# Kernel tuning notes

Hardware: AMD Instinct MI355X
Metric: run time of the kernel (lower is better)

## Reference

```python
import jax, jax.numpy as jnp
import numpy as np

B, NU, NI, D, L = 8, 1024, 2048, 64, 2
NUM_USERS, NUM_ITEMS = 100000, 50000


def setup_inputs() -> dict:
    key = jax.random.key(0)
    ks = jax.random.split(key, 9)
    return {
        "user_indices": jax.random.randint(ks[0], (B, NU), 0, NUM_USERS),
        "item_indices": jax.random.randint(ks[1], (B, NI), 0, NUM_ITEMS),
        "adj_matrices": jax.random.uniform(ks[2], (B, NU + NI, NU + NI), dtype=jnp.float32),
        "user_table": jax.random.normal(ks[3], (NUM_USERS, D), dtype=jnp.float32),
        "item_table": jax.random.normal(ks[4], (NUM_ITEMS, D), dtype=jnp.float32),
        "gc_w": jax.random.normal(ks[5], (L, D, D), dtype=jnp.float32) * 0.05,
        "gc_b": jax.random.normal(ks[6], (L, D), dtype=jnp.float32) * 0.05,
        "bi_w": jax.random.normal(ks[7], (L, D, D), dtype=jnp.float32) * 0.05,
        "bi_b": jax.random.normal(ks[8], (L, D), dtype=jnp.float32) * 0.05,
    }


def reference(user_indices, item_indices, adj_matrices, user_table, item_table, gc_w, gc_b, bi_w, bi_b):
    n_layers = gc_w.shape[0]

    def per_sample(u_idx, i_idx, adj):
        u_emb = user_table[u_idx]            # [NU, D]
        i_emb = item_table[i_idx]            # [NI, D]
        ego = jnp.concatenate([u_emb, i_emb], axis=0)  # [N, D]
        all_embs = [ego]
        for l in range(n_layers):
            side = adj @ ego                                        # [N, D]
            s = jax.nn.leaky_relu(side @ gc_w[l].T + gc_b[l])       # Linear(out,in) -> x @ W.T + b
            bi = jax.nn.leaky_relu((ego * side) @ bi_w[l].T + bi_b[l])
            ego = s + bi
            all_embs.append(ego)
        all_e = jnp.concatenate(all_embs, axis=1)                   # [N, D*(L+1)]
        u_g, i_g = all_e[: u_emb.shape[0]], all_e[u_emb.shape[0]:]
        scores = u_g @ i_g.T                                        # [NU, NI]
        return jax.nn.log_softmax(scores, axis=1)

    return jax.vmap(per_sample)(user_indices, item_indices, adj_matrices)
```

## Files before the change

kernel.cpp:

```cpp
#include <hip/hip_runtime.h>
#include <cstddef>

#define BB   8
#define NUU  1024
#define NII  2048
#define NTOT 3072
#define DD   64
#define KCAT 192

typedef __attribute__((ext_vector_type(8))) short bf16x8;
typedef __attribute__((ext_vector_type(4))) float f32x4;

__device__ __forceinline__ unsigned short f2bf(float f) {
  unsigned u = __float_as_uint(f);
  return (unsigned short)((u + 0x7fffu + ((u >> 16) & 1u)) >> 16);
}
__device__ __forceinline__ float bf2f(unsigned short s) {
  return __uint_as_float(((unsigned)s) << 16);
}
__device__ __forceinline__ uint4 pack8(float4 a, float4 b) {
  uint4 r;
  r.x = (unsigned)f2bf(a.x) | ((unsigned)f2bf(a.y) << 16);
  r.y = (unsigned)f2bf(a.z) | ((unsigned)f2bf(a.w) << 16);
  r.z = (unsigned)f2bf(b.x) | ((unsigned)f2bf(b.y) << 16);
  r.w = (unsigned)f2bf(b.z) | ((unsigned)f2bf(b.w) << 16);
  return r;
}
__device__ __forceinline__ bf16x8 u4_to_bf(uint4 u) {
  union { uint4 a; bf16x8 b; } x; x.a = u; return x.b;
}

__global__ __launch_bounds__(256) void transpose_w(
    const float* __restrict__ gcw, const float* __restrict__ biw,
    float* __restrict__ wT) {
  int g = blockIdx.x * 256 + threadIdx.x;
  int m = g >> 12, r = g & 4095;
  int k = r >> 6, d = r & 63;
  const float* src = (m < 2) ? gcw + m * 4096 : biw + (m - 2) * 4096;
  wT[g] = src[d * 64 + k];
}

__global__ __launch_bounds__(256) void gather_bf16(
    const int* __restrict__ uidx, const int* __restrict__ iidx,
    const float* __restrict__ utab, const float* __restrict__ itab,
    unsigned short* __restrict__ ecat) {
  int g = blockIdx.x * 256 + threadIdx.x;
  int node_g = g >> 2;
  int f0 = (g & 3) * 16;
  int b = node_g / NTOT;
  int row = node_g - b * NTOT;
  const float* src = (row < NUU) ? utab + (size_t)uidx[b * NUU + row] * DD
                                 : itab + (size_t)iidx[b * NII + row - NUU] * DD;
  const float4* s4 = reinterpret_cast<const float4*>(src + f0);
  uint4 lo = pack8(s4[0], s4[1]);
  uint4 hi = pack8(s4[2], s4[3]);
  uint4* dst = reinterpret_cast<uint4*>(ecat + (size_t)node_g * KCAT + f0);
  dst[0] = lo; dst[1] = hi;
}

__global__ __launch_bounds__(256) void conv_t(
    const unsigned short* __restrict__ ecat, int c0,
    unsigned short* __restrict__ Et) {
  __shared__ unsigned short T[64][65];
  const int tid = threadIdx.x;
  const int b = blockIdx.y;
  const int r0 = blockIdx.x * 64;
  {
    int nl = tid >> 2, fg = (tid & 3) * 16;
    const uint4* src = reinterpret_cast<const uint4*>(
        ecat + ((size_t)b * NTOT + r0 + nl) * KCAT + c0 + fg);
    uint4 v0 = src[0], v1 = src[1];
    unsigned short tmp[16];
    *reinterpret_cast<uint4*>(tmp) = v0;
    *reinterpret_cast<uint4*>(tmp + 8) = v1;
#pragma unroll
    for (int j = 0; j < 16; j++) T[fg + j][nl] = tmp[j];
  }
  __syncthreads();
  {
    int f = tid >> 2, ng = (tid & 3) * 16;
    unsigned short tmp[16];
#pragma unroll
    for (int j = 0; j < 16; j++) tmp[j] = T[f][ng + j];
    uint4* dst = reinterpret_cast<uint4*>(
        Et + ((size_t)b * DD + f) * NTOT + r0 + ng);
    dst[0] = *reinterpret_cast<uint4*>(tmp);
    dst[1] = *reinterpret_cast<uint4*>(tmp + 8);
  }
}

template <int CONV>
__global__ __launch_bounds__(256) void side_mfma_t(
    const float* __restrict__ adj, unsigned short* __restrict__ adjb,
    const unsigned short* __restrict__ Et, float* __restrict__ sp) {
  __shared__ __align__(16) unsigned short Bs[2][64][68];
  const int tid = threadIdx.x;
  const int w = tid >> 6, l = tid & 63;
  const int lane15 = l & 15, quad = l >> 4;
  const int b = blockIdx.z, kz = blockIdx.y;
  const int m0 = blockIdx.x * 64 + w * 16;
  const int kbase = kz * 768;
  const size_t rowoff = (size_t)b * NTOT * NTOT +
                        (size_t)(m0 + lane15) * NTOT + kbase + quad * 8;
  const float* A32 = adj + rowoff;
  const unsigned short* A16 = adjb + rowoff;
  unsigned short* Aw = adjb + rowoff;

  const int sf = tid >> 3, ss = (tid & 7) * 8;
  const unsigned short* Eb = Et + (size_t)b * DD * NTOT + kbase;
  uint4 p0 = *reinterpret_cast<const uint4*>(Eb + (size_t)sf * NTOT + ss);
  uint4 p1 = *reinterpret_cast<const uint4*>(Eb + (size_t)(sf + 32) * NTOT + ss);

  bf16x8 a0, a1;
  float4 f0, f1, f2, f3;
  if (CONV) {
    f0 = *reinterpret_cast<const float4*>(A32 + 0);
    f1 = *reinterpret_cast<const float4*>(A32 + 4);
    f2 = *reinterpret_cast<const float4*>(A32 + 32);
    f3 = *reinterpret_cast<const float4*>(A32 + 36);
  } else {
    a0 = *reinterpret_cast<const bf16x8*>(A16);
    a1 = *reinterpret_cast<const bf16x8*>(A16 + 32);
  }

  f32x4 acc[4];
#pragma unroll
  for (int t = 0; t < 4; t++) acc[t] = (f32x4){0.f, 0.f, 0.f, 0.f};

  for (int c = 0; c < 12; c++) {
    const int buf = c & 1;
    __syncthreads();
    *reinterpret_cast<uint4*>(&Bs[buf][sf][ss]) = p0;
    *reinterpret_cast<uint4*>(&Bs[buf][sf + 32][ss]) = p1;
    __syncthreads();

    if (CONV) {
      uint4 u0 = pack8(f0, f1), u1 = pack8(f2, f3);
      *reinterpret_cast<uint4*>(Aw + c * 64) = u0;
      *reinterpret_cast<uint4*>(Aw + c * 64 + 32) = u1;
      a0 = u4_to_bf(u0);
      a1 = u4_to_bf(u1);
    }

    bf16x8 na0, na1;
    if (c + 1 < 12) {
      p0 = *reinterpret_cast<const uint4*>(Eb + (size_t)sf * NTOT + (c + 1) * 64 + ss);
      p1 = *reinterpret_cast<const uint4*>(Eb + (size_t)(sf + 32) * NTOT + (c + 1) * 64 + ss);
      if (CONV) {
        f0 = *reinterpret_cast<const float4*>(A32 + (c + 1) * 64);
        f1 = *reinterpret_cast<const float4*>(A32 + (c + 1) * 64 + 4);
        f2 = *reinterpret_cast<const float4*>(A32 + (c + 1) * 64 + 32);
        f3 = *reinterpret_cast<const float4*>(A32 + (c + 1) * 64 + 36);
      } else {
        na0 = *reinterpret_cast<const bf16x8*>(A16 + (c + 1) * 64);
        na1 = *reinterpret_cast<const bf16x8*>(A16 + (c + 1) * 64 + 32);
      }
    }

#pragma unroll
    for (int t = 0; t < 4; t++) {
      bf16x8 b0 = *reinterpret_cast<const bf16x8*>(&Bs[buf][t * 16 + lane15][quad * 8]);
      acc[t] = __builtin_amdgcn_mfma_f32_16x16x32_bf16(a0, b0, acc[t], 0, 0, 0);
    }
#pragma unroll
    for (int t = 0; t < 4; t++) {
      bf16x8 b1 = *reinterpret_cast<const bf16x8*>(&Bs[buf][t * 16 + lane15][32 + quad * 8]);
      acc[t] = __builtin_amdgcn_mfma_f32_16x16x32_bf16(a1, b1, acc[t], 0, 0, 0);
    }
    if (!CONV && (c + 1 < 12)) { a0 = na0; a1 = na1; }
  }

  float* S = sp + ((size_t)kz * BB + b) * ((size_t)NTOT * DD);
#pragma unroll
  for (int t = 0; t < 4; t++)
#pragma unroll
    for (int r = 0; r < 4; r++)
      S[(size_t)(m0 + quad * 4 + r) * DD + t * 16 + lane15] = acc[t][r];
}

__global__ __launch_bounds__(256) void layer_post(
    const float* __restrict__ sp, unsigned short* __restrict__ ecat, int cin,
    const float* __restrict__ wTg, const float* __restrict__ wTb,
    const float* __restrict__ gcb, const float* __restrict__ bib) {
  __shared__ float wG[4096];
  __shared__ float wB[4096];
  __shared__ float rowS[4][64];
  __shared__ float rowE[4][64];
  const int tid = threadIdx.x;
#pragma unroll
  for (int i = 0; i < 16; i++) {
    int idx = tid + i * 256;
    wG[idx] = wTg[idx];
    wB[idx] = wTb[idx];
  }
  const int wv = tid >> 6, lane = tid & 63;
  const size_t row = (size_t)blockIdx.x * 4 + wv;
  const size_t off = row * DD + lane;
  const size_t P = (size_t)BB * NTOT * DD;
  float sv = sp[off] + sp[P + off] + sp[2 * P + off] + sp[3 * P + off];
  float ev = bf2f(ecat[row * KCAT + cin + lane]);
  rowS[wv][lane] = sv;
  rowE[wv][lane] = ev;
  __syncthreads();
  float sacc = gcb[lane];
  float bacc = bib[lane];
#pragma unroll 8
  for (int k = 0; k < 64; k++) {
    float sk = rowS[wv][k];
    float ek = rowE[wv][k];
    sacc += sk * wG[k * 64 + lane];
    bacc += (ek * sk) * wB[k * 64 + lane];
  }
  float s  = sacc > 0.f ? sacc : 0.01f * sacc;
  float bi = bacc > 0.f ? bacc : 0.01f * bacc;
  ecat[row * KCAT + cin + 64 + lane] = f2bf(s + bi);
}

__global__ __launch_bounds__(256) void scores_mfma(
    const unsigned short* __restrict__ ecat, float* __restrict__ out) {
  __shared__ __align__(16) unsigned short Ut[64 * KCAT];
  __shared__ __align__(16) unsigned short It[64 * KCAT];
  const int tid = threadIdx.x;
  const int w = tid >> 6, l = tid & 63;
  const int lane15 = l & 15, quad = l >> 4;
  const int b = blockIdx.z;
  const int u0 = blockIdx.y * 64;
  const int i0 = blockIdx.x * 64;
#pragma unroll
  for (int it = 0; it < 6; it++) {
    int idx = tid + it * 256;
    int row = idx / 24, c = idx - row * 24;
    int cs = c ^ (row & 7);
    uint4 vu = reinterpret_cast<const uint4*>(
        ecat + ((size_t)b * NTOT + u0 + row) * KCAT)[c];
    uint4 vi = reinterpret_cast<const uint4*>(
        ecat + ((size_t)b * NTOT + NUU + i0 + row) * KCAT)[c];
    reinterpret_cast<uint4*>(Ut)[row * 24 + cs] = vu;
    reinterpret_cast<uint4*>(It)[row * 24 + cs] = vi;
  }
  __syncthreads();
  f32x4 acc[4];
#pragma unroll
  for (int t = 0; t < 4; t++) acc[t] = (f32x4){0.f, 0.f, 0.f, 0.f};
  const int urow = w * 16 + lane15;
#pragma unroll
  for (int ks = 0; ks < 6; ks++) {
    int cu = (ks * 4 + quad) ^ (urow & 7);
    bf16x8 af = reinterpret_cast<const bf16x8*>(Ut)[urow * 24 + cu];
#pragma unroll
    for (int t = 0; t < 4; t++) {
      int irow = t * 16 + lane15;
      int ci = (ks * 4 + quad) ^ (irow & 7);
      bf16x8 bf = reinterpret_cast<const bf16x8*>(It)[irow * 24 + ci];
      acc[t] = __builtin_amdgcn_mfma_f32_16x16x32_bf16(af, bf, acc[t], 0, 0, 0);
    }
  }
  float* O = out + (size_t)b * NUU * NII;
#pragma unroll
  for (int t = 0; t < 4; t++)
#pragma unroll
    for (int r = 0; r < 4; r++)
      O[(size_t)(u0 + w * 16 + quad * 4 + r) * NII + i0 + t * 16 + lane15] =
          acc[t][r];
}

__global__ __launch_bounds__(256) void logsoftmax_kernel(float* __restrict__ out) {
  __shared__ float rm[4];
  __shared__ float rs[4];
  const int tid = threadIdx.x;
  const int lane = tid & 63, wv = tid >> 6;
  float* row = out + (size_t)blockIdx.x * NII;
  float4 v0 = *reinterpret_cast<const float4*>(row + tid * 4);
  float4 v1 = *reinterpret_cast<const float4*>(row + 1024 + tid * 4);
  float m = fmaxf(fmaxf(fmaxf(v0.x, v0.y), fmaxf(v0.z, v0.w)),
                  fmaxf(fmaxf(v1.x, v1.y), fmaxf(v1.z, v1.w)));
#pragma unroll
  for (int off = 32; off > 0; off >>= 1) m = fmaxf(m, __shfl_xor(m, off));
  if (lane == 0) rm[wv] = m;
  __syncthreads();
  m = fmaxf(fmaxf(rm[0], rm[1]), fmaxf(rm[2], rm[3]));
  float s = expf(v0.x - m) + expf(v0.y - m) + expf(v0.z - m) + expf(v0.w - m) +
            expf(v1.x - m) + expf(v1.y - m) + expf(v1.z - m) + expf(v1.w - m);
#pragma unroll
  for (int off = 32; off > 0; off >>= 1) s += __shfl_xor(s, off);
  if (lane == 0) rs[wv] = s;
  __syncthreads();
  float lse = m + logf(rs[0] + rs[1] + rs[2] + rs[3]);
  v0.x -= lse; v0.y -= lse; v0.z -= lse; v0.w -= lse;
  v1.x -= lse; v1.y -= lse; v1.z -= lse; v1.w -= lse;
  *reinterpret_cast<float4*>(row + tid * 4) = v0;
  *reinterpret_cast<float4*>(row + 1024 + tid * 4) = v1;
}

extern "C" void kernel_launch(void* const* d_in, const int* in_sizes, int n_in,
                              void* d_out, int out_size, void* d_ws, size_t ws_size,
                              hipStream_t stream) {
  (void)in_sizes; (void)n_in; (void)out_size; (void)ws_size;
  const int*   uidx = (const int*)d_in[0];
  const int*   iidx = (const int*)d_in[1];
  const float* adj  = (const float*)d_in[2];
  const float* utab = (const float*)d_in[3];
  const float* itab = (const float*)d_in[4];
  const float* gcw  = (const float*)d_in[5];
  const float* gcb  = (const float*)d_in[6];
  const float* biw  = (const float*)d_in[7];
  const float* bib  = (const float*)d_in[8];
  float* out = (float*)d_out;

  unsigned short* ecat = (unsigned short*)d_ws;
  unsigned short* Et   = ecat + (size_t)BB * NTOT * KCAT;
  unsigned short* adjb = Et + (size_t)BB * DD * NTOT;
  float* sp = (float*)d_out;
  const size_t P = (size_t)BB * NTOT * DD;
  float* wT = (float*)d_out + 4 * P;

  transpose_w<<<dim3(64), 256, 0, stream>>>(gcw, biw, wT);
  gather_bf16<<<dim3(BB * NTOT * 4 / 256), 256, 0, stream>>>(uidx, iidx, utab, itab, ecat);
  conv_t<<<dim3(48, BB), 256, 0, stream>>>(ecat, 0, Et);
  side_mfma_t<1><<<dim3(48, 4, BB), 256, 0, stream>>>(adj, adjb, Et, sp);
  layer_post<<<dim3(BB * NTOT / 4), 256, 0, stream>>>(sp, ecat, 0, wT, wT + 2 * 4096, gcb, bib);
  conv_t<<<dim3(48, BB), 256, 0, stream>>>(ecat, 64, Et);
  side_mfma_t<0><<<dim3(48, 4, BB), 256, 0, stream>>>(adj, adjb, Et, sp);
  layer_post<<<dim3(BB * NTOT / 4), 256, 0, stream>>>(sp, ecat, 64, wT + 4096, wT + 3 * 4096, gcb + 64, bib + 64);
  scores_mfma<<<dim3(32, 16, BB), 256, 0, stream>>>(ecat, out);
  logsoftmax_kernel<<<dim3(BB * NUU), 256, 0, stream>>>(out);
}
```

Measured before the change: 629.3 us.

## Fuse gather, transpose and weight prep; halve split-K; batch rows in layer_post

The embedding gather, the first bf16 transpose and the weight transpose now run in one kernel, which removes two launches and one round trip of ecat through global memory. The side GEMM's split-K factor drops from 4 to 2, so each block covers twice as many K chunks and fewer partial sums are written and reduced, at the cost of fewer blocks and longer serial loops. layer_post now handles 16 rows per block, four per wave, so the shared-memory weights are loaded fewer times and each weight read is reused across four rows.

```diff
diff --git a/kernel.cpp b/kernel.cpp
--- a/kernel.cpp
+++ b/kernel.cpp
@@ -30,32 +30,52 @@
   union { uint4 a; bf16x8 b; } x; x.a = u; return x.b;
 }
 
-__global__ __launch_bounds__(256) void transpose_w(
-    const float* __restrict__ gcw, const float* __restrict__ biw,
-    float* __restrict__ wT) {
-  int g = blockIdx.x * 256 + threadIdx.x;
-  int m = g >> 12, r = g & 4095;
-  int k = r >> 6, d = r & 63;
-  const float* src = (m < 2) ? gcw + m * 4096 : biw + (m - 2) * 4096;
-  wT[g] = src[d * 64 + k];
-}
-
-__global__ __launch_bounds__(256) void gather_bf16(
+__global__ __launch_bounds__(256) void gather_t(
     const int* __restrict__ uidx, const int* __restrict__ iidx,
     const float* __restrict__ utab, const float* __restrict__ itab,
-    unsigned short* __restrict__ ecat) {
-  int g = blockIdx.x * 256 + threadIdx.x;
-  int node_g = g >> 2;
-  int f0 = (g & 3) * 16;
-  int b = node_g / NTOT;
-  int row = node_g - b * NTOT;
-  const float* src = (row < NUU) ? utab + (size_t)uidx[b * NUU + row] * DD
-                                 : itab + (size_t)iidx[b * NII + row - NUU] * DD;
-  const float4* s4 = reinterpret_cast<const float4*>(src + f0);
-  uint4 lo = pack8(s4[0], s4[1]);
-  uint4 hi = pack8(s4[2], s4[3]);
-  uint4* dst = reinterpret_cast<uint4*>(ecat + (size_t)node_g * KCAT + f0);
-  dst[0] = lo; dst[1] = hi;
+    const float* __restrict__ gcw, const float* __restrict__ biw,
+    unsigned short* __restrict__ ecat, unsigned short* __restrict__ Et,
+    float* __restrict__ wT) {
+  const int tid = threadIdx.x;
+  if (blockIdx.x >= 384) {
+    for (int i = tid; i < 16384; i += 256) {
+      int m = i >> 12, r = i & 4095;
+      int k = r >> 6, d = r & 63;
+      const float* src = (m < 2) ? gcw + m * 4096 : biw + (m - 2) * 4096;
+      wT[i] = src[d * 64 + k];
+    }
+    return;
+  }
+  __shared__ unsigned short T[64][65];
+  const int b = blockIdx.x / 48;
+  const int r0 = (blockIdx.x % 48) * 64;
+  {
+    int nl = tid >> 2, f0 = (tid & 3) * 16;
+    int row = r0 + nl;
+    const float* src = (row < NUU) ? utab + (size_t)uidx[b * NUU + row] * DD
+                                   : itab + (size_t)iidx[b * NII + row - NUU] * DD;
+    const float4* s4 = reinterpret_cast<const float4*>(src + f0);
+    uint4 lo = pack8(s4[0], s4[1]);
+    uint4 hi = pack8(s4[2], s4[3]);
+    uint4* dst = reinterpret_cast<uint4*>(ecat + ((size_t)b * NTOT + row) * KCAT + f0);
+    dst[0] = lo; dst[1] = hi;
+    unsigned short tmp[16];
+    *reinterpret_cast<uint4*>(tmp) = lo;
+    *reinterpret_cast<uint4*>(tmp + 8) = hi;
+#pragma unroll
+    for (int j = 0; j < 16; j++) T[f0 + j][nl] = tmp[j];
+  }
+  __syncthreads();
+  {
+    int f = tid >> 2, ng = (tid & 3) * 16;
+    unsigned short tmp[16];
+#pragma unroll
+    for (int j = 0; j < 16; j++) tmp[j] = T[f][ng + j];
+    uint4* dst = reinterpret_cast<uint4*>(
+        Et + ((size_t)b * DD + f) * NTOT + r0 + ng);
+    dst[0] = *reinterpret_cast<uint4*>(tmp);
+    dst[1] = *reinterpret_cast<uint4*>(tmp + 8);
+  }
 }
 
 __global__ __launch_bounds__(256) void conv_t(
@@ -99,7 +119,7 @@
   const int lane15 = l & 15, quad = l >> 4;
   const int b = blockIdx.z, kz = blockIdx.y;
   const int m0 = blockIdx.x * 64 + w * 16;
-  const int kbase = kz * 768;
+  const int kbase = kz * 1536;
   const size_t rowoff = (size_t)b * NTOT * NTOT +
                         (size_t)(m0 + lane15) * NTOT + kbase + quad * 8;
   const float* A32 = adj + rowoff;
@@ -127,7 +147,7 @@
 #pragma unroll
   for (int t = 0; t < 4; t++) acc[t] = (f32x4){0.f, 0.f, 0.f, 0.f};
 
-  for (int c = 0; c < 12; c++) {
+  for (int c = 0; c < 24; c++) {
     const int buf = c & 1;
     __syncthreads();
     *reinterpret_cast<uint4*>(&Bs[buf][sf][ss]) = p0;
@@ -143,7 +163,7 @@
     }
 
     bf16x8 na0, na1;
-    if (c + 1 < 12) {
+    if (c + 1 < 24) {
       p0 = *reinterpret_cast<const uint4*>(Eb + (size_t)sf * NTOT + (c + 1) * 64 + ss);
       p1 = *reinterpret_cast<const uint4*>(Eb + (size_t)(sf + 32) * NTOT + (c + 1) * 64 + ss);
       if (CONV) {
@@ -167,7 +187,7 @@
       bf16x8 b1 = *reinterpret_cast<const bf16x8*>(&Bs[buf][t * 16 + lane15][32 + quad * 8]);
       acc[t] = __builtin_amdgcn_mfma_f32_16x16x32_bf16(a1, b1, acc[t], 0, 0, 0);
     }
-    if (!CONV && (c + 1 < 12)) { a0 = na0; a1 = na1; }
+    if (!CONV && (c + 1 < 24)) { a0 = na0; a1 = na1; }
   }
 
   float* S = sp + ((size_t)kz * BB + b) * ((size_t)NTOT * DD);
@@ -184,8 +204,8 @@
     const float* __restrict__ gcb, const float* __restrict__ bib) {
   __shared__ float wG[4096];
   __shared__ float wB[4096];
-  __shared__ float rowS[4][64];
-  __shared__ float rowE[4][64];
+  __shared__ float rowS[16][64];
+  __shared__ float rowE[16][64];
   const int tid = threadIdx.x;
 #pragma unroll
   for (int i = 0; i < 16; i++) {
@@ -194,26 +214,38 @@
     wB[idx] = wTb[idx];
   }
   const int wv = tid >> 6, lane = tid & 63;
-  const size_t row = (size_t)blockIdx.x * 4 + wv;
-  const size_t off = row * DD + lane;
+  const size_t base = (size_t)blockIdx.x * 16;
   const size_t P = (size_t)BB * NTOT * DD;
-  float sv = sp[off] + sp[P + off] + sp[2 * P + off] + sp[3 * P + off];
-  float ev = bf2f(ecat[row * KCAT + cin + lane]);
-  rowS[wv][lane] = sv;
-  rowE[wv][lane] = ev;
-  __syncthreads();
-  float sacc = gcb[lane];
-  float bacc = bib[lane];
+#pragma unroll
+  for (int rr = 0; rr < 4; rr++) {
+    const size_t row = base + wv * 4 + rr;
+    const size_t off = row * DD + lane;
+    rowS[wv * 4 + rr][lane] = sp[off] + sp[P + off];
+    rowE[wv * 4 + rr][lane] = bf2f(ecat[row * KCAT + cin + lane]);
+  }
+  __syncthreads();
+  float sacc[4], bacc[4];
+#pragma unroll
+  for (int rr = 0; rr < 4; rr++) { sacc[rr] = gcb[lane]; bacc[rr] = bib[lane]; }
 #pragma unroll 8
   for (int k = 0; k < 64; k++) {
-    float sk = rowS[wv][k];
-    float ek = rowE[wv][k];
-    sacc += sk * wG[k * 64 + lane];
-    bacc += (ek * sk) * wB[k * 64 + lane];
-  }
-  float s  = sacc > 0.f ? sacc : 0.01f * sacc;
-  float bi = bacc > 0.f ? bacc : 0.01f * bacc;
-  ecat[row * KCAT + cin + 64 + lane] = f2bf(s + bi);
+    float wg = wG[k * 64 + lane];
+    float wb = wB[k * 64 + lane];
+#pragma unroll
+    for (int rr = 0; rr < 4; rr++) {
+      float sk = rowS[wv * 4 + rr][k];
+      float ek = rowE[wv * 4 + rr][k];
+      sacc[rr] += sk * wg;
+      bacc[rr] += (ek * sk) * wb;
+    }
+  }
+#pragma unroll
+  for (int rr = 0; rr < 4; rr++) {
+    float s  = sacc[rr] > 0.f ? sacc[rr] : 0.01f * sacc[rr];
+    float bi = bacc[rr] > 0.f ? bacc[rr] : 0.01f * bacc[rr];
+    const size_t row = base + wv * 4 + rr;
+    ecat[row * KCAT + cin + 64 + lane] = f2bf(s + bi);
+  }
 }
 
 __global__ __launch_bounds__(256) void scores_mfma(
@@ -312,16 +344,14 @@
   unsigned short* adjb = Et + (size_t)BB * DD * NTOT;
   float* sp = (float*)d_out;
   const size_t P = (size_t)BB * NTOT * DD;
-  float* wT = (float*)d_out + 4 * P;
-
-  transpose_w<<<dim3(64), 256, 0, stream>>>(gcw, biw, wT);
-  gather_bf16<<<dim3(BB * NTOT * 4 / 256), 256, 0, stream>>>(uidx, iidx, utab, itab, ecat);
-  conv_t<<<dim3(48, BB), 256, 0, stream>>>(ecat, 0, Et);
-  side_mfma_t<1><<<dim3(48, 4, BB), 256, 0, stream>>>(adj, adjb, Et, sp);
-  layer_post<<<dim3(BB * NTOT / 4), 256, 0, stream>>>(sp, ecat, 0, wT, wT + 2 * 4096, gcb, bib);
+  float* wT = (float*)d_out + 2 * P;
+
+  gather_t<<<dim3(385), 256, 0, stream>>>(uidx, iidx, utab, itab, gcw, biw, ecat, Et, wT);
+  side_mfma_t<1><<<dim3(48, 2, BB), 256, 0, stream>>>(adj, adjb, Et, sp);
+  layer_post<<<dim3(BB * NTOT / 16), 256, 0, stream>>>(sp, ecat, 0, wT, wT + 2 * 4096, gcb, bib);
   conv_t<<<dim3(48, BB), 256, 0, stream>>>(ecat, 64, Et);
-  side_mfma_t<0><<<dim3(48, 4, BB), 256, 0, stream>>>(adj, adjb, Et, sp);
-  layer_post<<<dim3(BB * NTOT / 4), 256, 0, stream>>>(sp, ecat, 64, wT + 4096, wT + 3 * 4096, gcb + 64, bib + 64);
+  side_mfma_t<0><<<dim3(48, 2, BB), 256, 0, stream>>>(adj, adjb, Et, sp);
+  layer_post<<<dim3(BB * NTOT / 16), 256, 0, stream>>>(sp, ecat, 64, wT + 4096, wT + 3 * 4096, gcb + 64, bib + 64);
   scores_mfma<<<dim3(32, 16, BB), 256, 0, stream>>>(ecat, out);
   logsoftmax_kernel<<<dim3(BB * NUU), 256, 0, stream>>>(out);
 }
```

Result: faster. 605.1 us (-3.9%).
